# Kernel tuning notes

Measured on AMD Instinct MI355X. Metric: run time of the kernel, lower is better.

Reference implementation:

```python
import jax, jax.numpy as jnp
import numpy as np

N, C, H, W = 4, 256, 64, 64
C_EMBED = C // 2  # 128

def setup_inputs() -> dict:
    key = jax.random.key(0)
    k1, k2, k3, k4 = jax.random.split(key, 4)
    x = jax.random.normal(k1, (N, C, H, W), dtype=jnp.float32)
    # 1x1 conv weights stored as [out_ch, in_ch] (torch Conv2d weight squeezed)
    theta_w = jax.random.normal(k2, (C_EMBED, C), dtype=jnp.float32) * 0.01
    phi_w = jax.random.normal(k3, (C_EMBED, C), dtype=jnp.float32) * 0.01
    proj_w = jax.random.normal(k4, (C, C), dtype=jnp.float32) * 0.01
    return {"x": x, "theta_w": theta_w, "phi_w": phi_w, "proj_w": proj_w}

def reference(x, theta_w, phi_w, proj_w):
    n, c, h, w = x.shape
    s = h * w
    xf = x.reshape(n, c, s)  # [n, c, s]
    theta = jnp.einsum('ec,ncs->nse', theta_w, xf)  # [n, s, e]
    phi = jnp.einsum('ec,ncs->nes', phi_w, xf)      # [n, e, s]
    scale = jnp.sqrt(jnp.float32(theta_w.shape[0]))
    f = jnp.einsum('nse,net->nst', theta, phi) / scale  # [n, s, s]
    f = jax.nn.softmax(f, axis=-1)
    y = jnp.einsum('nst,nct->ncs', f, xf)  # attend over g = x, -> [n, c, s]
    res = jnp.einsum('oc,ncs->nos', proj_w, y)  # 1x1 projection conv
    return x + res.reshape(n, c, h, w)
```

## Files before the change

kernel.cpp:

```cpp
#include <hip/hip_runtime.h>
#include <cstdint>
#include <cstddef>

#define NB 4
#define CH 256
#define SS 4096
#define EE 128
#define QSCALE 0.08838834764831845f

typedef __attribute__((ext_vector_type(8))) short bfrag;
typedef __attribute__((ext_vector_type(8))) unsigned short u16x8;
typedef __attribute__((ext_vector_type(4))) float f32x4;

__device__ __forceinline__ unsigned short f2bf(float f) {
  union { float f; unsigned int u; } v; v.f = f;
  unsigned int u = v.u;
  unsigned int r = u + 0x7FFFu + ((u >> 16) & 1u);
  return (unsigned short)(r >> 16);
}

__global__ __launch_bounds__(256) void cvt_all(
    const float* __restrict__ x,   const float* __restrict__ thw,
    const float* __restrict__ phw, const float* __restrict__ pw,
    unsigned short* __restrict__ xb,   unsigned short* __restrict__ thwb,
    unsigned short* __restrict__ phwb, unsigned short* __restrict__ pwb)
{
  const int nx4 = NB * CH * SS / 4;
  const int nw4 = EE * CH / 4;
  const int np4 = CH * CH / 4;
  int i = blockIdx.x * 256 + threadIdx.x;
  const float* src; unsigned short* dst; int off;
  if      (i < nx4)                 { src = x;   dst = xb;   off = i; }
  else if (i < nx4 + nw4)           { src = thw; dst = thwb; off = i - nx4; }
  else if (i < nx4 + 2 * nw4)       { src = phw; dst = phwb; off = i - nx4 - nw4; }
  else if (i < nx4 + 2 * nw4 + np4) { src = pw;  dst = pwb;  off = i - nx4 - 2 * nw4; }
  else return;
  float4 v = reinterpret_cast<const float4*>(src)[off];
  ushort4 o;
  o.x = f2bf(v.x); o.y = f2bf(v.y); o.z = f2bf(v.z); o.w = f2bf(v.w);
  reinterpret_cast<ushort4*>(dst)[off] = o;
}

__global__ __launch_bounds__(256) void pass1_qk(
    const unsigned short* __restrict__ xb,
    const unsigned short* __restrict__ thw,
    const unsigned short* __restrict__ phw,
    unsigned short* __restrict__ Qt,
    unsigned short* __restrict__ Kt)
{
  __shared__ unsigned short xT[64][CH + 8];
  const int t  = threadIdx.x;
  const int n  = blockIdx.y;
  const int s0 = blockIdx.x * 64;
  const int z  = blockIdx.z;

  {
    const int soff = (t & 15) * 4;
    const int c0   = t >> 4;
    const ushort4* xv = reinterpret_cast<const ushort4*>(
        xb + ((size_t)n * CH) * SS + s0);
    #pragma unroll
    for (int ci = 0; ci < 16; ++ci) {
      const int c = c0 + ci * 16;
      ushort4 v = xv[c * (SS / 4) + (soff >> 2)];
      xT[soff + 0][c] = v.x;
      xT[soff + 1][c] = v.y;
      xT[soff + 2][c] = v.z;
      xT[soff + 3][c] = v.w;
    }
  }
  __syncthreads();

  const int w    = t >> 6;
  const int lane = t & 63;
  const int q    = lane >> 4;
  const int mr   = lane & 15;

  bfrag a[8];
  {
    const bfrag* rp = reinterpret_cast<const bfrag*>(&xT[w * 16 + mr][0]);
    #pragma unroll
    for (int k = 0; k < 8; ++k) a[k] = rp[k * 4 + q];
  }

  const unsigned short* wsel = z ? phw : thw;
  unsigned short*       osel = z ? Kt  : Qt;
  const float           sc   = z ? 1.0f : QSCALE;
  const bfrag* wp = reinterpret_cast<const bfrag*>(wsel);
  #pragma unroll
  for (int nt = 0; nt < 8; ++nt) {
    f32x4 acc = {0.f, 0.f, 0.f, 0.f};
    #pragma unroll
    for (int k = 0; k < 8; ++k) {
      bfrag b = wp[(nt * 16 + mr) * (CH / 8) + k * 4 + q];
      acc = __builtin_amdgcn_mfma_f32_16x16x32_bf16(a[k], b, acc, 0, 0, 0);
    }
    #pragma unroll
    for (int i = 0; i < 4; ++i) {
      const int srow = s0 + w * 16 + q * 4 + i;
      osel[((size_t)n * SS + srow) * EE + nt * 16 + mr] = f2bf(acc[i] * sc);
    }
  }
}

__global__ __launch_bounds__(512, 2) void pass2_attn(
    const unsigned short* __restrict__ Qt,
    const unsigned short* __restrict__ Kt,
    const unsigned short* __restrict__ xb,
    unsigned short* __restrict__ Yt)
{
  __shared__ float          S_lds[64][132];
  __shared__ unsigned short P_lds[64][136];
  __shared__ float row_m[64], row_l[64], row_alpha[64];

  const int t    = threadIdx.x;
  const int n    = blockIdx.y;
  const int s0   = blockIdx.x * 64;
  const int w    = t >> 6;
  const int lane = t & 63;
  const int q    = lane >> 4;
  const int mr   = lane & 15;

  if (t < 64) { row_m[t] = -INFINITY; row_l[t] = 0.f; }

  bfrag qa[4][4];
  #pragma unroll
  for (int ms = 0; ms < 4; ++ms) {
    const bfrag* rp = reinterpret_cast<const bfrag*>(
        Qt + ((size_t)n * SS + s0 + ms * 16 + mr) * EE);
    #pragma unroll
    for (int k = 0; k < 4; ++k) qa[ms][k] = rp[k * 4 + q];
  }

  f32x4 o_acc[4][2];
  #pragma unroll
  for (int ms = 0; ms < 4; ++ms)
    #pragma unroll
    for (int nt = 0; nt < 2; ++nt) o_acc[ms][nt] = (f32x4){0.f, 0.f, 0.f, 0.f};

  bfrag kb[4];
  {
    const bfrag* rp = reinterpret_cast<const bfrag*>(
        Kt + ((size_t)n * SS + w * 16 + mr) * EE);
    #pragma unroll
    for (int k = 0; k < 4; ++k) kb[k] = rp[k * 4 + q];
  }

  for (int t0 = 0; t0 < SS; t0 += 128) {
    bfrag vb[4][2];
    #pragma unroll
    for (int nt = 0; nt < 2; ++nt) {
      const int c = w * 32 + nt * 16 + mr;
      const bfrag* vp = reinterpret_cast<const bfrag*>(
          xb + ((size_t)n * CH + c) * SS + t0);
      #pragma unroll
      for (int kk = 0; kk < 4; ++kk) vb[kk][nt] = vp[kk * 4 + q];
    }

    #pragma unroll
    for (int ms = 0; ms < 4; ++ms) {
      f32x4 acc = {0.f, 0.f, 0.f, 0.f};
      #pragma unroll
      for (int k = 0; k < 4; ++k)
        acc = __builtin_amdgcn_mfma_f32_16x16x32_bf16(qa[ms][k], kb[k], acc, 0, 0, 0);
      #pragma unroll
      for (int i = 0; i < 4; ++i)
        S_lds[ms * 16 + q * 4 + i][w * 16 + mr] = acc[i];
    }
    __syncthreads();

    {
      const int t1 = t0 + 128;
      if (t1 < SS) {
        const bfrag* rp = reinterpret_cast<const bfrag*>(
            Kt + ((size_t)n * SS + t1 + w * 16 + mr) * EE);
        #pragma unroll
        for (int k = 0; k < 4; ++k) kb[k] = rp[k * 4 + q];
      }
    }

    {
      const int r  = t >> 3;
      const int cg = t & 7;
      const float4* srow = reinterpret_cast<const float4*>(&S_lds[r][cg * 16]);
      float4 v0 = srow[0], v1 = srow[1], v2 = srow[2], v3 = srow[3];
      float vmax = fmaxf(fmaxf(fmaxf(v0.x, v0.y), fmaxf(v0.z, v0.w)),
                         fmaxf(fmaxf(v1.x, v1.y), fmaxf(v1.z, v1.w)));
      vmax = fmaxf(vmax, fmaxf(fmaxf(fmaxf(v2.x, v2.y), fmaxf(v2.z, v2.w)),
                               fmaxf(fmaxf(v3.x, v3.y), fmaxf(v3.z, v3.w))));
      vmax = fmaxf(vmax, __shfl_xor(vmax, 1, 8));
      vmax = fmaxf(vmax, __shfl_xor(vmax, 2, 8));
      vmax = fmaxf(vmax, __shfl_xor(vmax, 4, 8));
      const float m_old = row_m[r];
      const float m_new = fmaxf(m_old, vmax);

      float p[16];
      p[0]=__expf(v0.x-m_new); p[1]=__expf(v0.y-m_new); p[2]=__expf(v0.z-m_new); p[3]=__expf(v0.w-m_new);
      p[4]=__expf(v1.x-m_new); p[5]=__expf(v1.y-m_new); p[6]=__expf(v1.z-m_new); p[7]=__expf(v1.w-m_new);
      p[8]=__expf(v2.x-m_new); p[9]=__expf(v2.y-m_new); p[10]=__expf(v2.z-m_new); p[11]=__expf(v2.w-m_new);
      p[12]=__expf(v3.x-m_new); p[13]=__expf(v3.y-m_new); p[14]=__expf(v3.z-m_new); p[15]=__expf(v3.w-m_new);
      float sum = 0.f;
      u16x8 pk0, pk1;
      #pragma unroll
      for (int j = 0; j < 8; ++j) { sum += p[j];     pk0[j] = f2bf(p[j]); }
      #pragma unroll
      for (int j = 0; j < 8; ++j) { sum += p[8 + j]; pk1[j] = f2bf(p[8 + j]); }
      *reinterpret_cast<u16x8*>(&P_lds[r][cg * 16])     = pk0;
      *reinterpret_cast<u16x8*>(&P_lds[r][cg * 16 + 8]) = pk1;
      sum += __shfl_xor(sum, 1, 8);
      sum += __shfl_xor(sum, 2, 8);
      sum += __shfl_xor(sum, 4, 8);
      if (cg == 0) {
        const float al = __expf(m_old - m_new);
        row_alpha[r] = al;
        row_m[r]     = m_new;
        row_l[r]     = row_l[r] * al + sum;
      }
    }
    __syncthreads();

    #pragma unroll
    for (int ms = 0; ms < 4; ++ms) {
      float al[4];
      #pragma unroll
      for (int i = 0; i < 4; ++i) al[i] = row_alpha[ms * 16 + q * 4 + i];
      #pragma unroll
      for (int nt = 0; nt < 2; ++nt)
        #pragma unroll
        for (int i = 0; i < 4; ++i) o_acc[ms][nt][i] *= al[i];
    }

    #pragma unroll
    for (int kk = 0; kk < 4; ++kk) {
      bfrag pa[4];
      #pragma unroll
      for (int ms = 0; ms < 4; ++ms)
        pa[ms] = reinterpret_cast<const bfrag*>(&P_lds[ms * 16 + mr][0])[kk * 4 + q];
      #pragma unroll
      for (int nt = 0; nt < 2; ++nt)
        #pragma unroll
        for (int ms = 0; ms < 4; ++ms)
          o_acc[ms][nt] = __builtin_amdgcn_mfma_f32_16x16x32_bf16(
              pa[ms], vb[kk][nt], o_acc[ms][nt], 0, 0, 0);
    }
  }

  #pragma unroll
  for (int ms = 0; ms < 4; ++ms) {
    float inv[4];
    #pragma unroll
    for (int i = 0; i < 4; ++i) inv[i] = 1.0f / row_l[ms * 16 + q * 4 + i];
    #pragma unroll
    for (int nt = 0; nt < 2; ++nt) {
      const int c = w * 32 + nt * 16 + mr;
      #pragma unroll
      for (int i = 0; i < 4; ++i) {
        const int s = s0 + ms * 16 + q * 4 + i;
        Yt[((size_t)n * SS + s) * CH + c] = f2bf(o_acc[ms][nt][i] * inv[i]);
      }
    }
  }
}

__global__ __launch_bounds__(256) void pass3_proj(
    const unsigned short* __restrict__ Yt,
    const unsigned short* __restrict__ pw,
    const float* __restrict__ x,
    float* __restrict__ out)
{
  const int t    = threadIdx.x;
  const int w    = t >> 6;
  const int lane = t & 63;
  const int q    = lane >> 4;
  const int mr   = lane & 15;
  const int n    = blockIdx.z;
  const int o0   = blockIdx.y * 64 + w * 16;
  const int s1   = blockIdx.x * 64;

  bfrag a[8];
  {
    const bfrag* ap = reinterpret_cast<const bfrag*>(pw + (o0 + mr) * CH);
    #pragma unroll
    for (int k = 0; k < 8; ++k) a[k] = ap[k * 4 + q];
  }

  #pragma unroll
  for (int nt = 0; nt < 4; ++nt) {
    f32x4 acc = {0.f, 0.f, 0.f, 0.f};
    const bfrag* bp = reinterpret_cast<const bfrag*>(
        Yt + ((size_t)n * SS + s1 + nt * 16 + mr) * CH);
    #pragma unroll
    for (int k = 0; k < 8; ++k)
      acc = __builtin_amdgcn_mfma_f32_16x16x32_bf16(a[k], bp[k * 4 + q], acc, 0, 0, 0);
    #pragma unroll
    for (int i = 0; i < 4; ++i) {
      const int o = o0 + q * 4 + i;
      const int s = s1 + nt * 16 + mr;
      const size_t idx = ((size_t)n * CH + o) * SS + s;
      out[idx] = x[idx] + acc[i];
    }
  }
}

extern "C" void kernel_launch(void* const* d_in, const int* in_sizes, int n_in,
                              void* d_out, int out_size, void* d_ws, size_t ws_size,
                              hipStream_t stream) {
  const float* x   = (const float*)d_in[0];
  const float* thw = (const float*)d_in[1];
  const float* phw = (const float*)d_in[2];
  const float* pw  = (const float*)d_in[3];
  float* out = (float*)d_out;

  unsigned short* xb   = (unsigned short*)d_ws;
  unsigned short* Yt   = xb + (size_t)NB * CH * SS;
  unsigned short* Qt   = Yt + (size_t)NB * CH * SS;
  unsigned short* Kt   = Qt + (size_t)NB * SS * EE;
  unsigned short* thwb = Kt + (size_t)NB * SS * EE;
  unsigned short* phwb = thwb + EE * CH;
  unsigned short* pwb  = phwb + EE * CH;

  const int nx4 = NB * CH * SS / 4;
  const int nw4 = EE * CH / 4;
  const int np4 = CH * CH / 4;
  const int tot4 = nx4 + 2 * nw4 + np4;
  cvt_all<<<(tot4 + 255) / 256, 256, 0, stream>>>(
      x, thw, phw, pw, xb, thwb, phwb, pwb);

  pass1_qk  <<<dim3(SS / 64, NB, 2),       256, 0, stream>>>(xb, thwb, phwb, Qt, Kt);
  pass2_attn<<<dim3(SS / 64, NB),          512, 0, stream>>>(Qt, Kt, xb, Yt);
  pass3_proj<<<dim3(SS / 64, CH / 64, NB), 256, 0, stream>>>(Yt, pwb, x, out);
}
```

Measured before the change: 215.7 us.

## Split attention key range in two and merge partial softmax results in projection

The attention kernel now splits the key/value sequence into two halves along a new grid dimension, writing per-split normalized outputs plus row max and sum to workspace. The projection kernel combines the two partial outputs with log-sum-exp weights before its MFMA. This doubles the attention grid from 256 to 512 blocks to fill more compute units on the GPU. The cost is extra workspace traffic for two bf16 output copies and an added rounding step in the merge.

```diff
diff --git a/kernel.cpp b/kernel.cpp
--- a/kernel.cpp
+++ b/kernel.cpp
@@ -6,6 +6,8 @@
 #define CH 256
 #define SS 4096
 #define EE 128
+#define NSPLIT 2
+#define KLEN (SS / NSPLIT)
 #define QSCALE 0.08838834764831845f
 
 typedef __attribute__((ext_vector_type(8))) short bfrag;
@@ -17,6 +19,10 @@
   unsigned int u = v.u;
   unsigned int r = u + 0x7FFFu + ((u >> 16) & 1u);
   return (unsigned short)(r >> 16);
+}
+__device__ __forceinline__ float bf2f(unsigned short h) {
+  union { unsigned int u; float f; } v; v.u = ((unsigned int)h) << 16;
+  return v.f;
 }
 
 __global__ __launch_bounds__(256) void cvt_all(
@@ -107,7 +113,9 @@
     const unsigned short* __restrict__ Qt,
     const unsigned short* __restrict__ Kt,
     const unsigned short* __restrict__ xb,
-    unsigned short* __restrict__ Yt)
+    unsigned short* __restrict__ Osp,
+    float* __restrict__ Msp,
+    float* __restrict__ Lsp)
 {
   __shared__ float          S_lds[64][132];
   __shared__ unsigned short P_lds[64][136];
@@ -116,6 +124,8 @@
   const int t    = threadIdx.x;
   const int n    = blockIdx.y;
   const int s0   = blockIdx.x * 64;
+  const int z    = blockIdx.z;
+  const int tbeg = z * KLEN;
   const int w    = t >> 6;
   const int lane = t & 63;
   const int q    = lane >> 4;
@@ -141,12 +151,12 @@
   bfrag kb[4];
   {
     const bfrag* rp = reinterpret_cast<const bfrag*>(
-        Kt + ((size_t)n * SS + w * 16 + mr) * EE);
+        Kt + ((size_t)n * SS + tbeg + w * 16 + mr) * EE);
     #pragma unroll
     for (int k = 0; k < 4; ++k) kb[k] = rp[k * 4 + q];
   }
 
-  for (int t0 = 0; t0 < SS; t0 += 128) {
+  for (int t0 = tbeg; t0 < tbeg + KLEN; t0 += 128) {
     bfrag vb[4][2];
     #pragma unroll
     for (int nt = 0; nt < 2; ++nt) {
@@ -171,7 +181,7 @@
 
     {
       const int t1 = t0 + 128;
-      if (t1 < SS) {
+      if (t1 < tbeg + KLEN) {
         const bfrag* rp = reinterpret_cast<const bfrag*>(
             Kt + ((size_t)n * SS + t1 + w * 16 + mr) * EE);
         #pragma unroll
@@ -256,18 +266,28 @@
       #pragma unroll
       for (int i = 0; i < 4; ++i) {
         const int s = s0 + ms * 16 + q * 4 + i;
-        Yt[((size_t)n * SS + s) * CH + c] = f2bf(o_acc[ms][nt][i] * inv[i]);
+        Osp[((size_t)(n * NSPLIT + z) * SS + s) * CH + c] =
+            f2bf(o_acc[ms][nt][i] * inv[i]);
       }
     }
   }
+  if (t < 64) {
+    const size_t mi = (size_t)(n * NSPLIT + z) * SS + s0 + t;
+    Msp[mi] = row_m[t];
+    Lsp[mi] = row_l[t];
+  }
 }
 
 __global__ __launch_bounds__(256) void pass3_proj(
-    const unsigned short* __restrict__ Yt,
+    const unsigned short* __restrict__ Osp,
+    const float* __restrict__ Msp,
+    const float* __restrict__ Lsp,
     const unsigned short* __restrict__ pw,
     const float* __restrict__ x,
     float* __restrict__ out)
 {
+  __shared__ float wn0[64], wn1[64];
+
   const int t    = threadIdx.x;
   const int w    = t >> 6;
   const int lane = t & 63;
@@ -277,6 +297,21 @@
   const int o0   = blockIdx.y * 64 + w * 16;
   const int s1   = blockIdx.x * 64;
 
+  if (t < 64) {
+    const int s = s1 + t;
+    const size_t i0 = (size_t)(n * NSPLIT + 0) * SS + s;
+    const size_t i1 = (size_t)(n * NSPLIT + 1) * SS + s;
+    const float m0 = Msp[i0], m1 = Msp[i1];
+    const float l0 = Lsp[i0], l1 = Lsp[i1];
+    const float m  = fmaxf(m0, m1);
+    const float a0 = __expf(m0 - m) * l0;
+    const float a1 = __expf(m1 - m) * l1;
+    const float inv = 1.0f / (a0 + a1);
+    wn0[t] = a0 * inv;
+    wn1[t] = a1 * inv;
+  }
+  __syncthreads();
+
   bfrag a[8];
   {
     const bfrag* ap = reinterpret_cast<const bfrag*>(pw + (o0 + mr) * CH);
@@ -286,12 +321,25 @@
 
   #pragma unroll
   for (int nt = 0; nt < 4; ++nt) {
+    const int srow = s1 + nt * 16 + mr;
+    const float w0 = wn0[nt * 16 + mr];
+    const float w1 = wn1[nt * 16 + mr];
+    const bfrag* bp0 = reinterpret_cast<const bfrag*>(
+        Osp + ((size_t)(n * NSPLIT + 0) * SS + srow) * CH);
+    const bfrag* bp1 = reinterpret_cast<const bfrag*>(
+        Osp + ((size_t)(n * NSPLIT + 1) * SS + srow) * CH);
     f32x4 acc = {0.f, 0.f, 0.f, 0.f};
-    const bfrag* bp = reinterpret_cast<const bfrag*>(
-        Yt + ((size_t)n * SS + s1 + nt * 16 + mr) * CH);
-    #pragma unroll
-    for (int k = 0; k < 8; ++k)
-      acc = __builtin_amdgcn_mfma_f32_16x16x32_bf16(a[k], bp[k * 4 + q], acc, 0, 0, 0);
+    #pragma unroll
+    for (int k = 0; k < 8; ++k) {
+      bfrag b0 = bp0[k * 4 + q];
+      bfrag b1 = bp1[k * 4 + q];
+      bfrag bb;
+      #pragma unroll
+      for (int j = 0; j < 8; ++j)
+        bb[j] = (short)f2bf(w0 * bf2f((unsigned short)b0[j]) +
+                            w1 * bf2f((unsigned short)b1[j]));
+      acc = __builtin_amdgcn_mfma_f32_16x16x32_bf16(a[k], bb, acc, 0, 0, 0);
+    }
     #pragma unroll
     for (int i = 0; i < 4; ++i) {
       const int o = o0 + q * 4 + i;
@@ -312,12 +360,14 @@
   float* out = (float*)d_out;
 
   unsigned short* xb   = (unsigned short*)d_ws;
-  unsigned short* Yt   = xb + (size_t)NB * CH * SS;
-  unsigned short* Qt   = Yt + (size_t)NB * CH * SS;
+  unsigned short* Osp  = xb + (size_t)NB * CH * SS;
+  unsigned short* Qt   = Osp + (size_t)NSPLIT * NB * SS * CH;
   unsigned short* Kt   = Qt + (size_t)NB * SS * EE;
   unsigned short* thwb = Kt + (size_t)NB * SS * EE;
   unsigned short* phwb = thwb + EE * CH;
   unsigned short* pwb  = phwb + EE * CH;
+  float*          Msp  = (float*)(pwb + CH * CH);
+  float*          Lsp  = Msp + (size_t)NSPLIT * NB * SS;
 
   const int nx4 = NB * CH * SS / 4;
   const int nw4 = EE * CH / 4;
@@ -327,6 +377,6 @@
       x, thw, phw, pw, xb, thwb, phwb, pwb);
 
   pass1_qk  <<<dim3(SS / 64, NB, 2),       256, 0, stream>>>(xb, thwb, phwb, Qt, Kt);
-  pass2_attn<<<dim3(SS / 64, NB),          512, 0, stream>>>(Qt, Kt, xb, Yt);
-  pass3_proj<<<dim3(SS / 64, CH / 64, NB), 256, 0, stream>>>(Yt, pwb, x, out);
-}
+  pass2_attn<<<dim3(SS / 64, NB, NSPLIT),  512, 0, stream>>>(Qt, Kt, xb, Osp, Msp, Lsp);
+  pass3_proj<<<dim3(SS / 64, CH / 64, NB), 256, 0, stream>>>(Osp, Msp, Lsp, pwb, x, out);
+}
```

Measured after the change: 234.6 us. 8.8% more time.
